# Kernel optimization log

Hardware: AMD Instinct MI355X
Metric: run time of the kernel (lower is better)

## Reference

```python
import jax, jax.numpy as jnp
import numpy as np

N_HEAD = 16
N_EMBD = 1024
B, T = 4, 2048


def setup_inputs() -> dict:
    key = jax.random.key(0)
    k1, k2, k3, k4, k5 = jax.random.split(key, 5)
    x = jax.random.normal(k1, (B, T, N_EMBD), dtype=jnp.float32)
    # Linear params (torch nn.Linear: y = x @ W.T + b); store as [in, out] for einsum
    s = 1.0 / np.sqrt(N_EMBD)
    W_qkv = jax.random.uniform(k2, (N_EMBD, 3 * N_EMBD), minval=-s, maxval=s, dtype=jnp.float32)
    b_qkv = jax.random.uniform(k3, (3 * N_EMBD,), minval=-s, maxval=s, dtype=jnp.float32)
    W_out = jax.random.uniform(k4, (N_EMBD, N_EMBD), minval=-s, maxval=s, dtype=jnp.float32)
    b_out = jax.random.uniform(k5, (N_EMBD,), minval=-s, maxval=s, dtype=jnp.float32)
    return {"x": x, "W_qkv": W_qkv, "b_qkv": b_qkv, "W_out": W_out, "b_out": b_out}


def reference(x, W_qkv, b_qkv, W_out, b_out):
    Bv, Tv, C = x.shape
    H = N_HEAD
    d_k = C // H
    qkv = x @ W_qkv + b_qkv                      # [B,T,3C]
    q, k, v = jnp.split(qkv, 3, axis=-1)
    # [B,T,C] -> [B,H,T,d_k]
    def to_heads(t):
        return t.reshape(Bv, Tv, H, d_k).transpose(0, 2, 1, 3)
    q, k, v = to_heads(q), to_heads(k), to_heads(v)
    scores = jnp.einsum('bhqd,bhkd->bhqk', q, k) / jnp.sqrt(jnp.float32(d_k))
    causal = jnp.tril(jnp.ones((Tv, Tv), dtype=bool))  # True = keep
    scores = jnp.where(causal, scores, jnp.float32(-jnp.inf))
    attn = jax.nn.softmax(scores, axis=-1)
    out = jnp.einsum('bhqk,bhkd->bhqd', attn, v)       # [B,H,T,d_k]
    out = out.transpose(0, 2, 1, 3).reshape(Bv, Tv, C)
    return out @ W_out + b_out
```

## Files before the change

kernel.cpp:

```cpp
#include <hip/hip_runtime.h>

#define T_SEQ 2048
#define NBATCH 4
#define NHEAD 16
#define DKH 64
#define CEMB 1024

typedef unsigned short u16;
typedef __attribute__((ext_vector_type(8))) short short8;
typedef __attribute__((ext_vector_type(8))) unsigned short ushort8v;
typedef __attribute__((ext_vector_type(4))) float f32x4;

__device__ __forceinline__ u16 f2bf(float f) {
  unsigned int x = __builtin_bit_cast(unsigned int, f);
  x += 0x7FFFu + ((x >> 16) & 1u);
  return (u16)(x >> 16);
}

__device__ __forceinline__ void async_copy16(const void* g, void* lds) {
  __builtin_amdgcn_global_load_lds(
      (const __attribute__((address_space(1))) void*)g,
      (__attribute__((address_space(3))) void*)lds, 16, 0, 0);
}

__global__ __launch_bounds__(256) void k_convert(const float* __restrict__ in,
                                                 u16* __restrict__ out, int n8) {
  int i = blockIdx.x * 256 + threadIdx.x;
  if (i >= n8) return;
  const float4* p = (const float4*)in;
  float4 a = p[2 * i], b = p[2 * i + 1];
  ushort8v v;
  v[0] = f2bf(a.x); v[1] = f2bf(a.y); v[2] = f2bf(a.z); v[3] = f2bf(a.w);
  v[4] = f2bf(b.x); v[5] = f2bf(b.y); v[6] = f2bf(b.z); v[7] = f2bf(b.w);
  ((ushort8v*)out)[i] = v;
}

__global__ __launch_bounds__(256) void k_transpose(const float* __restrict__ W,
                                                   u16* __restrict__ WT, int R, int C) {
  __shared__ float tile[32][33];
  int c0 = blockIdx.x * 32, r0 = blockIdx.y * 32;
  int tx = threadIdx.x & 31;
  int ty = threadIdx.x >> 5;
#pragma unroll
  for (int i = 0; i < 4; ++i) {
    int r = ty + i * 8;
    tile[r][tx] = W[(size_t)(r0 + r) * C + c0 + tx];
  }
  __syncthreads();
#pragma unroll
  for (int i = 0; i < 4; ++i) {
    int cc = ty + i * 8;
    WT[(size_t)(c0 + cc) * R + r0 + tx] = f2bf(tile[tx][cc]);
  }
}

template <int EPI>
__global__ __launch_bounds__(256) void k_gemm_bt(
    const u16* __restrict__ A, const u16* __restrict__ BT, const float* __restrict__ bias,
    float* __restrict__ Cf, u16* __restrict__ Qb, u16* __restrict__ Kb, u16* __restrict__ Vtb,
    int M, int N, int K) {
  __shared__ u16 As[128 * 32];
  __shared__ u16 Bs[128 * 32];
  const int tid = threadIdx.x;
  const int w = tid >> 6, l = tid & 63;
  const int g = l >> 4, lr = l & 15;
  const int m0 = blockIdx.y * 128, n0 = blockIdx.x * 128;
  const int wr = (w >> 1) * 64, wc = (w & 1) * 64;
  f32x4 acc[4][4] = {};

  const int srow = l >> 2;
  const int scol = (l & 3) << 3;
  const u16* Ag = A + (size_t)m0 * K + scol;
  const u16* Bg = BT + (size_t)n0 * K + scol;

  for (int k0 = 0; k0 < K; k0 += 32) {
#pragma unroll
    for (int i = 0; i < 2; ++i) {
      int blk = i * 4 + w;
      int row = blk * 16 + srow;
      async_copy16(Ag + (size_t)row * K + k0, &As[blk * 512]);
      async_copy16(Bg + (size_t)row * K + k0, &Bs[blk * 512]);
    }
    __syncthreads();
    short8 af[4], bf[4];
#pragma unroll
    for (int mi = 0; mi < 4; ++mi)
      af[mi] = *(const short8*)&As[(wr + mi * 16 + lr) * 32 + g * 8];
#pragma unroll
    for (int ni = 0; ni < 4; ++ni)
      bf[ni] = *(const short8*)&Bs[(wc + ni * 16 + lr) * 32 + g * 8];
#pragma unroll
    for (int mi = 0; mi < 4; ++mi)
#pragma unroll
      for (int ni = 0; ni < 4; ++ni)
        acc[mi][ni] = __builtin_amdgcn_mfma_f32_16x16x32_bf16(af[mi], bf[ni], acc[mi][ni], 0, 0, 0);
    __syncthreads();
  }

  if constexpr (EPI == 0) {
#pragma unroll
    for (int mi = 0; mi < 4; ++mi) {
#pragma unroll
      for (int ni = 0; ni < 4; ++ni) {
        int ng = n0 + wc + ni * 16 + lr;
        float bs = bias[ng];
#pragma unroll
        for (int r = 0; r < 4; ++r) {
          int mg = m0 + wr + mi * 16 + g * 4 + r;
          Cf[(size_t)mg * N + ng] = acc[mi][ni][r] + bs;
        }
      }
    }
  } else {
#pragma unroll
    for (int mi = 0; mi < 4; ++mi) {
      int mg0 = m0 + wr + mi * 16 + g * 4;
      int b = mg0 >> 11;
      int t = mg0 & (T_SEQ - 1);
#pragma unroll
      for (int ni = 0; ni < 4; ++ni) {
        int ng = n0 + wc + ni * 16 + lr;
        float bs = bias[ng];
        int sect = ng >> 10;
        int nm = ng & 1023;
        int h = nm >> 6, d = nm & 63;
        u16 bv[4];
#pragma unroll
        for (int r = 0; r < 4; ++r) bv[r] = f2bf(acc[mi][ni][r] + bs);
        size_t hb = (size_t)b * NHEAD + h;
        if (sect == 0) {
          u16* q = Qb + (hb * T_SEQ + t) * DKH + d;
#pragma unroll
          for (int r = 0; r < 4; ++r) q[(size_t)r * DKH] = bv[r];
        } else if (sect == 1) {
          u16* kk = Kb + (hb * T_SEQ + t) * DKH + d;
#pragma unroll
          for (int r = 0; r < 4; ++r) kk[(size_t)r * DKH] = bv[r];
        } else {
          u16* vp = Vtb + (hb * DKH + d) * T_SEQ + t;
          ushort4 v4;
          v4.x = bv[0]; v4.y = bv[1]; v4.z = bv[2]; v4.w = bv[3];
          *(ushort4*)vp = v4;
        }
      }
    }
  }
}

__global__ __launch_bounds__(256) void k_attn(const u16* __restrict__ Qb,
                                              const u16* __restrict__ Kb,
                                              const u16* __restrict__ Vtb,
                                              u16* __restrict__ Ob) {
  __shared__ u16 Ks[2][64 * 64];
  __shared__ u16 Vs[2][64 * 64];
  __shared__ u16 Ps[4][32 * 72];
  const int tid = threadIdx.x;
  const int w = tid >> 6, l = tid & 63;
  const int g = l >> 4, lr = l & 15;
  const int bh = blockIdx.y;
  const int b = bh >> 4, h = bh & 15;
  const int qt = (int)(gridDim.x - 1) - (int)blockIdx.x;
  const int q0 = qt * 128;
  const int q0w = q0 + w * 32;
  const u16* Qg = Qb + (size_t)bh * T_SEQ * DKH;
  const u16* Kg = Kb + (size_t)bh * T_SEQ * DKH;
  const u16* Vg = Vtb + (size_t)bh * DKH * T_SEQ;

  const u16* KgL[2];
  const u16* VgL[2];
  int blkArr[2];
#pragma unroll
  for (int i = 0; i < 2; ++i) {
    int blk = i * 4 + w;
    blkArr[i] = blk;
    int x = blk * 1024 + l * 16;
    int c = x ^ (((x >> 7) & 7) << 4);
    int crow = c >> 7;
    int ccolb = c & 127;
    KgL[i] = Kg + crow * DKH + (ccolb >> 1);
    VgL[i] = Vg + (size_t)crow * T_SEQ + (ccolb >> 1);
  }

  auto STAGE = [&](int bufi, int kv0) {
#pragma unroll
    for (int i = 0; i < 2; ++i) {
      async_copy16(KgL[i] + (size_t)kv0 * DKH, &Ks[bufi][blkArr[i] * 512]);
      async_copy16(VgL[i] + kv0, &Vs[bufi][blkArr[i] * 512]);
    }
  };

  STAGE(0, 0);

  short8 qfr[2][2];
#pragma unroll
  for (int qi = 0; qi < 2; ++qi)
#pragma unroll
    for (int ka = 0; ka < 2; ++ka)
      qfr[qi][ka] = *(const short8*)&Qg[(size_t)(q0w + qi * 16 + lr) * DKH + ka * 32 + g * 8];

  f32x4 o[2][4] = {};
  float m_[2][4], lp[2][4];
#pragma unroll
  for (int qi = 0; qi < 2; ++qi)
#pragma unroll
    for (int r = 0; r < 4; ++r) { m_[qi][r] = -1e30f; lp[qi][r] = 0.f; }

  __syncthreads();

  const int ntile = q0 / 64 + 2;
  for (int kt = 0; kt < ntile; ++kt) {
    const int cur = kt & 1;
    const int kv0 = kt * 64;
    if (kt + 1 < ntile) STAGE(cur ^ 1, kv0 + 64);

    if (kv0 <= q0w) {
      const bool diag = (kv0 + 63 > q0w);
      const char* KsB = (const char*)Ks[cur];
      const char* VsB = (const char*)Vs[cur];
      short8 kf[4][2];
#pragma unroll
      for (int kv = 0; kv < 4; ++kv)
#pragma unroll
        for (int ka = 0; ka < 2; ++ka) {
          int row = kv * 16 + lr;
          int cidx = row * 128 + ka * 64 + g * 16;
          int x = cidx ^ ((row & 7) << 4);
          kf[kv][ka] = *(const short8*)(KsB + x);
        }
      f32x4 s[2][4] = {};
      __builtin_amdgcn_s_setprio(1);
#pragma unroll
      for (int qi = 0; qi < 2; ++qi)
#pragma unroll
        for (int kv = 0; kv < 4; ++kv)
#pragma unroll
          for (int ka = 0; ka < 2; ++ka)
            s[qi][kv] = __builtin_amdgcn_mfma_f32_16x16x32_bf16(qfr[qi][ka], kf[kv][ka], s[qi][kv], 0, 0, 0);
      __builtin_amdgcn_s_setprio(0);

      if (diag) {
#pragma unroll
        for (int qi = 0; qi < 2; ++qi)
#pragma unroll
          for (int kv = 0; kv < 4; ++kv)
#pragma unroll
            for (int r = 0; r < 4; ++r) {
              int qq = q0w + qi * 16 + g * 4 + r;
              int kk = kv0 + kv * 16 + lr;
              if (kk > qq) s[qi][kv][r] = -1e30f;
            }
      }

      float pmx[2][4];
      bool grow = false;
#pragma unroll
      for (int qi = 0; qi < 2; ++qi)
#pragma unroll
        for (int r = 0; r < 4; ++r) {
          float v = fmaxf(fmaxf(s[qi][0][r], s[qi][1][r]), fmaxf(s[qi][2][r], s[qi][3][r]));
          pmx[qi][r] = v;
          grow = grow || (v > m_[qi][r] + 64.f);
        }
      if (__any(grow)) {
#pragma unroll
        for (int qi = 0; qi < 2; ++qi)
#pragma unroll
          for (int r = 0; r < 4; ++r) {
            float v = pmx[qi][r];
            v = fmaxf(v, __shfl_xor(v, 1));
            v = fmaxf(v, __shfl_xor(v, 2));
            v = fmaxf(v, __shfl_xor(v, 4));
            v = fmaxf(v, __shfl_xor(v, 8));
            float mn = fmaxf(m_[qi][r], v);
            float al = __expf((m_[qi][r] - mn) * 0.125f);
            m_[qi][r] = mn;
            lp[qi][r] *= al;
#pragma unroll
            for (int df = 0; df < 4; ++df) o[qi][df][r] *= al;
          }
      }

#pragma unroll
      for (int qi = 0; qi < 2; ++qi)
#pragma unroll
        for (int r = 0; r < 4; ++r) {
          float mm = m_[qi][r];
          float p0 = __expf((s[qi][0][r] - mm) * 0.125f);
          float p1 = __expf((s[qi][1][r] - mm) * 0.125f);
          float p2 = __expf((s[qi][2][r] - mm) * 0.125f);
          float p3 = __expf((s[qi][3][r] - mm) * 0.125f);
          lp[qi][r] += (p0 + p1) + (p2 + p3);
          u16* base = &Ps[w][(qi * 16 + g * 4 + r) * 72 + lr];
          base[0]  = f2bf(p0);
          base[16] = f2bf(p1);
          base[32] = f2bf(p2);
          base[48] = f2bf(p3);
        }

      short8 pf[2][2];
#pragma unroll
      for (int qi = 0; qi < 2; ++qi)
#pragma unroll
        for (int ka = 0; ka < 2; ++ka)
          pf[qi][ka] = *(const short8*)&Ps[w][(qi * 16 + lr) * 72 + ka * 32 + g * 8];
      short8 vf[4][2];
#pragma unroll
      for (int df = 0; df < 4; ++df)
#pragma unroll
        for (int ka = 0; ka < 2; ++ka) {
          int row = df * 16 + lr;
          int cidx = row * 128 + ka * 64 + g * 16;
          int x = cidx ^ ((row & 7) << 4);
          vf[df][ka] = *(const short8*)(VsB + x);
        }
      __builtin_amdgcn_s_setprio(1);
#pragma unroll
      for (int qi = 0; qi < 2; ++qi)
#pragma unroll
        for (int df = 0; df < 4; ++df)
#pragma unroll
          for (int ka = 0; ka < 2; ++ka)
            o[qi][df] = __builtin_amdgcn_mfma_f32_16x16x32_bf16(pf[qi][ka], vf[df][ka], o[qi][df], 0, 0, 0);
      __builtin_amdgcn_s_setprio(0);
    }

    __syncthreads();
  }

#pragma unroll
  for (int qi = 0; qi < 2; ++qi)
#pragma unroll
    for (int r = 0; r < 4; ++r) {
      float v = lp[qi][r];
      v += __shfl_xor(v, 1);
      v += __shfl_xor(v, 2);
      v += __shfl_xor(v, 4);
      v += __shfl_xor(v, 8);
      float inv = 1.0f / v;
      int tq = q0w + qi * 16 + g * 4 + r;
      size_t base = ((size_t)b * T_SEQ + tq) * CEMB + h * 64;
#pragma unroll
      for (int df = 0; df < 4; ++df)
        Ob[base + df * 16 + lr] = f2bf(o[qi][df][r] * inv);
    }
}

extern "C" void kernel_launch(void* const* d_in, const int* in_sizes, int n_in,
                              void* d_out, int out_size, void* d_ws, size_t ws_size,
                              hipStream_t stream) {
  const float* x = (const float*)d_in[0];
  const float* Wqkv = (const float*)d_in[1];
  const float* bqkv = (const float*)d_in[2];
  const float* Wout = (const float*)d_in[3];
  const float* bout = (const float*)d_in[4];
  float* out = (float*)d_out;

  char* ws = (char*)d_ws;
  u16* xb  = (u16*)(ws + 0);
  u16* WqT = (u16*)(ws + 16777216);
  u16* WoT = (u16*)(ws + 23068672);
  u16* Qb  = (u16*)(ws + 25165824);
  u16* Kb  = (u16*)(ws + 41943040);
  u16* Vtb = (u16*)(ws + 58720256);
  u16* Ob  = (u16*)(ws + 75497472);

  k_convert<<<4096, 256, 0, stream>>>(x, xb, (NBATCH * T_SEQ * CEMB) / 8);
  k_transpose<<<dim3(96, 32), 256, 0, stream>>>(Wqkv, WqT, 1024, 3072);
  k_transpose<<<dim3(32, 32), 256, 0, stream>>>(Wout, WoT, 1024, 1024);
  k_gemm_bt<1><<<dim3(24, 64), 256, 0, stream>>>(xb, WqT, bqkv, nullptr, Qb, Kb, Vtb,
                                                 NBATCH * T_SEQ, 3 * CEMB, CEMB);
  k_attn<<<dim3(16, 64), 256, 0, stream>>>(Qb, Kb, Vtb, Ob);
  k_gemm_bt<0><<<dim3(8, 64), 256, 0, stream>>>(Ob, WoT, bout, out, nullptr, nullptr, nullptr,
                                                NBATCH * T_SEQ, CEMB, CEMB);
}
```

Before: 355.5 us.

## Pair complementary causal query tiles per block to balance work and share K/V

```diff
diff --git a/kernel.cpp b/kernel.cpp
--- a/kernel.cpp
+++ b/kernel.cpp
@@ -147,10 +147,10 @@
   }
 }
 
-__global__ __launch_bounds__(256) void k_attn(const u16* __restrict__ Qb,
-                                              const u16* __restrict__ Kb,
-                                              const u16* __restrict__ Vtb,
-                                              u16* __restrict__ Ob) {
+__global__ __launch_bounds__(256, 2) void k_attn(const u16* __restrict__ Qb,
+                                                 const u16* __restrict__ Kb,
+                                                 const u16* __restrict__ Vtb,
+                                                 u16* __restrict__ Ob) {
   __shared__ u16 Ks[2][64 * 64];
   __shared__ u16 Vs[2][64 * 64];
   __shared__ u16 Ps[4][32 * 72];
@@ -159,9 +159,10 @@
   const int g = l >> 4, lr = l & 15;
   const int bh = blockIdx.y;
   const int b = bh >> 4, h = bh & 15;
-  const int qt = (int)(gridDim.x - 1) - (int)blockIdx.x;
-  const int q0 = qt * 128;
-  const int q0w = q0 + w * 32;
+  const int j = blockIdx.x;
+  const int qtB = 15 - j;
+  const int q0a = j * 128 + w * 32;
+  const int q0b = qtB * 128 + w * 32;
   const u16* Qg = Qb + (size_t)bh * T_SEQ * DKH;
   const u16* Kg = Kb + (size_t)bh * T_SEQ * DKH;
   const u16* Vg = Vtb + (size_t)bh * DKH * T_SEQ;
@@ -191,33 +192,128 @@
 
   STAGE(0, 0);
 
-  short8 qfr[2][2];
+  short8 qfrA[2][2], qfrB[2][2];
 #pragma unroll
   for (int qi = 0; qi < 2; ++qi)
 #pragma unroll
-    for (int ka = 0; ka < 2; ++ka)
-      qfr[qi][ka] = *(const short8*)&Qg[(size_t)(q0w + qi * 16 + lr) * DKH + ka * 32 + g * 8];
-
-  f32x4 o[2][4] = {};
-  float m_[2][4], lp[2][4];
+    for (int ka = 0; ka < 2; ++ka) {
+      qfrA[qi][ka] = *(const short8*)&Qg[(size_t)(q0a + qi * 16 + lr) * DKH + ka * 32 + g * 8];
+      qfrB[qi][ka] = *(const short8*)&Qg[(size_t)(q0b + qi * 16 + lr) * DKH + ka * 32 + g * 8];
+    }
+
+  f32x4 oA[2][4] = {}, oB[2][4] = {};
+  float mA[2][4], lpA[2][4], mB[2][4], lpB[2][4];
 #pragma unroll
   for (int qi = 0; qi < 2; ++qi)
 #pragma unroll
-    for (int r = 0; r < 4; ++r) { m_[qi][r] = -1e30f; lp[qi][r] = 0.f; }
+    for (int r = 0; r < 4; ++r) {
+      mA[qi][r] = -1e30f; lpA[qi][r] = 0.f;
+      mB[qi][r] = -1e30f; lpB[qi][r] = 0.f;
+    }
 
   __syncthreads();
 
-  const int ntile = q0 / 64 + 2;
+  short8 kf[4][2], vf[4][2];
+  auto tile_compute = [&](int q0w_, auto& qfr_, auto& o_, auto& m__, auto& lp_, int kv0) {
+    const bool diag = (kv0 + 63 > q0w_);
+    f32x4 s[2][4] = {};
+    __builtin_amdgcn_s_setprio(1);
+#pragma unroll
+    for (int qi = 0; qi < 2; ++qi)
+#pragma unroll
+      for (int kv = 0; kv < 4; ++kv)
+#pragma unroll
+        for (int ka = 0; ka < 2; ++ka)
+          s[qi][kv] = __builtin_amdgcn_mfma_f32_16x16x32_bf16(qfr_[qi][ka], kf[kv][ka], s[qi][kv], 0, 0, 0);
+    __builtin_amdgcn_s_setprio(0);
+
+    if (diag) {
+#pragma unroll
+      for (int qi = 0; qi < 2; ++qi)
+#pragma unroll
+        for (int kv = 0; kv < 4; ++kv)
+#pragma unroll
+          for (int r = 0; r < 4; ++r) {
+            int qq = q0w_ + qi * 16 + g * 4 + r;
+            int kk = kv0 + kv * 16 + lr;
+            if (kk > qq) s[qi][kv][r] = -1e30f;
+          }
+    }
+
+    float pmx[2][4];
+    bool grow = false;
+#pragma unroll
+    for (int qi = 0; qi < 2; ++qi)
+#pragma unroll
+      for (int r = 0; r < 4; ++r) {
+        float v = fmaxf(fmaxf(s[qi][0][r], s[qi][1][r]), fmaxf(s[qi][2][r], s[qi][3][r]));
+        pmx[qi][r] = v;
+        grow = grow || (v > m__[qi][r] + 64.f);
+      }
+    if (__any(grow)) {
+#pragma unroll
+      for (int qi = 0; qi < 2; ++qi)
+#pragma unroll
+        for (int r = 0; r < 4; ++r) {
+          float v = pmx[qi][r];
+          v = fmaxf(v, __shfl_xor(v, 1));
+          v = fmaxf(v, __shfl_xor(v, 2));
+          v = fmaxf(v, __shfl_xor(v, 4));
+          v = fmaxf(v, __shfl_xor(v, 8));
+          float mn = fmaxf(m__[qi][r], v);
+          float al = __expf((m__[qi][r] - mn) * 0.125f);
+          m__[qi][r] = mn;
+          lp_[qi][r] *= al;
+#pragma unroll
+          for (int df = 0; df < 4; ++df) o_[qi][df][r] *= al;
+        }
+    }
+
+#pragma unroll
+    for (int qi = 0; qi < 2; ++qi)
+#pragma unroll
+      for (int r = 0; r < 4; ++r) {
+        float mm = m__[qi][r];
+        float p0 = __expf((s[qi][0][r] - mm) * 0.125f);
+        float p1 = __expf((s[qi][1][r] - mm) * 0.125f);
+        float p2 = __expf((s[qi][2][r] - mm) * 0.125f);
+        float p3 = __expf((s[qi][3][r] - mm) * 0.125f);
+        lp_[qi][r] += (p0 + p1) + (p2 + p3);
+        u16* base = &Ps[w][(qi * 16 + g * 4 + r) * 72 + lr];
+        base[0]  = f2bf(p0);
+        base[16] = f2bf(p1);
+        base[32] = f2bf(p2);
+        base[48] = f2bf(p3);
+      }
+
+    short8 pf[2][2];
+#pragma unroll
+    for (int qi = 0; qi < 2; ++qi)
+#pragma unroll
+      for (int ka = 0; ka < 2; ++ka)
+        pf[qi][ka] = *(const short8*)&Ps[w][(qi * 16 + lr) * 72 + ka * 32 + g * 8];
+    __builtin_amdgcn_s_setprio(1);
+#pragma unroll
+    for (int qi = 0; qi < 2; ++qi)
+#pragma unroll
+      for (int df = 0; df < 4; ++df)
+#pragma unroll
+        for (int ka = 0; ka < 2; ++ka)
+          o_[qi][df] = __builtin_amdgcn_mfma_f32_16x16x32_bf16(pf[qi][ka], vf[df][ka], o_[qi][df], 0, 0, 0);
+    __builtin_amdgcn_s_setprio(0);
+  };
+
+  const int ntile = 2 * qtB + 2;
   for (int kt = 0; kt < ntile; ++kt) {
     const int cur = kt & 1;
     const int kv0 = kt * 64;
     if (kt + 1 < ntile) STAGE(cur ^ 1, kv0 + 64);
 
-    if (kv0 <= q0w) {
-      const bool diag = (kv0 + 63 > q0w);
+    const bool actA = (kv0 <= q0a);
+    const bool actB = (kv0 <= q0b);
+    if (actB) {
       const char* KsB = (const char*)Ks[cur];
       const char* VsB = (const char*)Vs[cur];
-      short8 kf[4][2];
 #pragma unroll
       for (int kv = 0; kv < 4; ++kv)
 #pragma unroll
@@ -226,122 +322,38 @@
           int cidx = row * 128 + ka * 64 + g * 16;
           int x = cidx ^ ((row & 7) << 4);
           kf[kv][ka] = *(const short8*)(KsB + x);
+          vf[kv][ka] = *(const short8*)(VsB + x);
         }
-      f32x4 s[2][4] = {};
-      __builtin_amdgcn_s_setprio(1);
-#pragma unroll
-      for (int qi = 0; qi < 2; ++qi)
-#pragma unroll
-        for (int kv = 0; kv < 4; ++kv)
-#pragma unroll
-          for (int ka = 0; ka < 2; ++ka)
-            s[qi][kv] = __builtin_amdgcn_mfma_f32_16x16x32_bf16(qfr[qi][ka], kf[kv][ka], s[qi][kv], 0, 0, 0);
-      __builtin_amdgcn_s_setprio(0);
-
-      if (diag) {
-#pragma unroll
-        for (int qi = 0; qi < 2; ++qi)
-#pragma unroll
-          for (int kv = 0; kv < 4; ++kv)
-#pragma unroll
-            for (int r = 0; r < 4; ++r) {
-              int qq = q0w + qi * 16 + g * 4 + r;
-              int kk = kv0 + kv * 16 + lr;
-              if (kk > qq) s[qi][kv][r] = -1e30f;
-            }
-      }
-
-      float pmx[2][4];
-      bool grow = false;
-#pragma unroll
-      for (int qi = 0; qi < 2; ++qi)
-#pragma unroll
-        for (int r = 0; r < 4; ++r) {
-          float v = fmaxf(fmaxf(s[qi][0][r], s[qi][1][r]), fmaxf(s[qi][2][r], s[qi][3][r]));
-          pmx[qi][r] = v;
-          grow = grow || (v > m_[qi][r] + 64.f);
-        }
-      if (__any(grow)) {
-#pragma unroll
-        for (int qi = 0; qi < 2; ++qi)
-#pragma unroll
-          for (int r = 0; r < 4; ++r) {
-            float v = pmx[qi][r];
-            v = fmaxf(v, __shfl_xor(v, 1));
-            v = fmaxf(v, __shfl_xor(v, 2));
-            v = fmaxf(v, __shfl_xor(v, 4));
-            v = fmaxf(v, __shfl_xor(v, 8));
-            float mn = fmaxf(m_[qi][r], v);
-            float al = __expf((m_[qi][r] - mn) * 0.125f);
-            m_[qi][r] = mn;
-            lp[qi][r] *= al;
-#pragma unroll
-            for (int df = 0; df < 4; ++df) o[qi][df][r] *= al;
-          }
-      }
-
-#pragma unroll
-      for (int qi = 0; qi < 2; ++qi)
-#pragma unroll
-        for (int r = 0; r < 4; ++r) {
-          float mm = m_[qi][r];
-          float p0 = __expf((s[qi][0][r] - mm) * 0.125f);
-          float p1 = __expf((s[qi][1][r] - mm) * 0.125f);
-          float p2 = __expf((s[qi][2][r] - mm) * 0.125f);
-          float p3 = __expf((s[qi][3][r] - mm) * 0.125f);
-          lp[qi][r] += (p0 + p1) + (p2 + p3);
-          u16* base = &Ps[w][(qi * 16 + g * 4 + r) * 72 + lr];
-          base[0]  = f2bf(p0);
-          base[16] = f2bf(p1);
-          base[32] = f2bf(p2);
-          base[48] = f2bf(p3);
-        }
-
-      short8 pf[2][2];
-#pragma unroll
-      for (int qi = 0; qi < 2; ++qi)
-#pragma unroll
-        for (int ka = 0; ka < 2; ++ka)
-          pf[qi][ka] = *(const short8*)&Ps[w][(qi * 16 + lr) * 72 + ka * 32 + g * 8];
-      short8 vf[4][2];
+      if (actA) tile_compute(q0a, qfrA, oA, mA, lpA, kv0);
+      tile_compute(q0b, qfrB, oB, mB, lpB, kv0);
+    }
+
+    __syncthreads();
+  }
+
+#pragma unroll
+  for (int qi = 0; qi < 2; ++qi)
+#pragma unroll
+    for (int r = 0; r < 4; ++r) {
+      float va = lpA[qi][r];
+      va += __shfl_xor(va, 1); va += __shfl_xor(va, 2);
+      va += __shfl_xor(va, 4); va += __shfl_xor(va, 8);
+      float inva = 1.0f / va;
+      int tqa = q0a + qi * 16 + g * 4 + r;
+      size_t basea = ((size_t)b * T_SEQ + tqa) * CEMB + h * 64;
 #pragma unroll
       for (int df = 0; df < 4; ++df)
-#pragma unroll
-        for (int ka = 0; ka < 2; ++ka) {
-          int row = df * 16 + lr;
-          int cidx = row * 128 + ka * 64 + g * 16;
-          int x = cidx ^ ((row & 7) << 4);
-          vf[df][ka] = *(const short8*)(VsB + x);
-        }
-      __builtin_amdgcn_s_setprio(1);
-#pragma unroll
-      for (int qi = 0; qi < 2; ++qi)
-#pragma unroll
-        for (int df = 0; df < 4; ++df)
-#pragma unroll
-          for (int ka = 0; ka < 2; ++ka)
-            o[qi][df] = __builtin_amdgcn_mfma_f32_16x16x32_bf16(pf[qi][ka], vf[df][ka], o[qi][df], 0, 0, 0);
-      __builtin_amdgcn_s_setprio(0);
-    }
-
-    __syncthreads();
-  }
-
-#pragma unroll
-  for (int qi = 0; qi < 2; ++qi)
-#pragma unroll
-    for (int r = 0; r < 4; ++r) {
-      float v = lp[qi][r];
-      v += __shfl_xor(v, 1);
-      v += __shfl_xor(v, 2);
-      v += __shfl_xor(v, 4);
-      v += __shfl_xor(v, 8);
-      float inv = 1.0f / v;
-      int tq = q0w + qi * 16 + g * 4 + r;
-      size_t base = ((size_t)b * T_SEQ + tq) * CEMB + h * 64;
+        Ob[basea + df * 16 + lr] = f2bf(oA[qi][df][r] * inva);
+
+      float vb = lpB[qi][r];
+      vb += __shfl_xor(vb, 1); vb += __shfl_xor(vb, 2);
+      vb += __shfl_xor(vb, 4); vb += __shfl_xor(vb, 8);
+      float invb = 1.0f / vb;
+      int tqb = q0b + qi * 16 + g * 4 + r;
+      size_t baseb = ((size_t)b * T_SEQ + tqb) * CEMB + h * 64;
 #pragma unroll
       for (int df = 0; df < 4; ++df)
-        Ob[base + df * 16 + lr] = f2bf(o[qi][df][r] * inv);
+        Ob[baseb + df * 16 + lr] = f2bf(oB[qi][df][r] * invb);
     }
 }
 
@@ -369,7 +381,7 @@
   k_transpose<<<dim3(32, 32), 256, 0, stream>>>(Wout, WoT, 1024, 1024);
   k_gemm_bt<1><<<dim3(24, 64), 256, 0, stream>>>(xb, WqT, bqkv, nullptr, Qb, Kb, Vtb,
                                                  NBATCH * T_SEQ, 3 * CEMB, CEMB);
-  k_attn<<<dim3(16, 64), 256, 0, stream>>>(Qb, Kb, Vtb, Ob);
+  k_attn<<<dim3(8, 64), 256, 0, stream>>>(Qb, Kb, Vtb, Ob);
   k_gemm_bt<0><<<dim3(8, 64), 256, 0, stream>>>(Ob, WoT, bout, out, nullptr, nullptr, nullptr,
                                                 NBATCH * T_SEQ, CEMB, CEMB);
 }
```

After: 294.1 us. 1.21x faster.
